# Kernel optimization log

Hardware: AMD Instinct MI355X
Metric: run time of the kernel (lower is better)

Reference implementation:

```python
import jax, jax.numpy as jnp
import numpy as np

N_USERS = 100000
N_MOVIES = 100000
N_EDGES = 1000000
HIDDEN = 128


def setup_inputs() -> dict:
    key = jax.random.key(0)
    k1, k2, k3, k4, k5, k6, k7 = jax.random.split(key, 7)
    user_features = jax.random.normal(k1, (N_USERS, HIDDEN), dtype=jnp.float32)
    movie_features = jax.random.normal(k2, (N_MOVIES, HIDDEN), dtype=jnp.float32)
    src = jax.random.randint(k3, (N_EDGES,), 0, N_USERS, dtype=jnp.int64 if jax.config.jax_enable_x64 else jnp.int32)
    dst = jax.random.randint(k4, (N_EDGES,), 0, N_MOVIES, dtype=jnp.int64 if jax.config.jax_enable_x64 else jnp.int32)
    edge_index = jnp.stack([src, dst], axis=0)
    # Linear(2*HIDDEN, HIDDEN) params, torch-style init (kaiming uniform ~ U(-1/sqrt(fan_in), 1/sqrt(fan_in)))
    b1_bound = 1.0 / np.sqrt(2 * HIDDEN)
    W1 = jax.random.uniform(k5, (2 * HIDDEN, HIDDEN), minval=-b1_bound, maxval=b1_bound, dtype=jnp.float32)
    b1 = jax.random.uniform(k6, (HIDDEN,), minval=-b1_bound, maxval=b1_bound, dtype=jnp.float32)
    b2_bound = 1.0 / np.sqrt(HIDDEN)
    k8, k9 = jax.random.split(k7)
    W2 = jax.random.uniform(k8, (HIDDEN, 1), minval=-b2_bound, maxval=b2_bound, dtype=jnp.float32)
    b2 = jax.random.uniform(k9, (1,), minval=-b2_bound, maxval=b2_bound, dtype=jnp.float32)
    return {"user_features": user_features, "movie_features": movie_features,
            "edge_index": edge_index, "W1": W1, "b1": b1, "W2": W2, "b2": b2}


def reference(user_features, movie_features, edge_index, W1, b1, W2, b2):
    # Gather endpoint features per edge: [E, H] each
    u = user_features[edge_index[0]]
    m = movie_features[edge_index[1]]
    edge_feats = jnp.concatenate([u, m], axis=1)  # [E, 2H]
    h = jax.nn.relu(edge_feats @ W1 + b1)         # [E, H]
    out = h @ W2 + b2                             # [E, 1]
    return out.reshape(-1)
```

## Files before the change

### kernel.cpp

```cpp
#include <hip/hip_runtime.h>
#include <hip/hip_bf16.h>

typedef short s8v __attribute__((ext_vector_type(8)));
typedef float f4v __attribute__((ext_vector_type(4)));

__device__ __forceinline__ unsigned int bfround(float f) {
    unsigned int x = __float_as_uint(f);
    return (x + 0x7fffu + ((x >> 16) & 1u)) >> 16;
}
__device__ __forceinline__ unsigned int pkbf(float x, float y) {
    __hip_bfloat162 h = __float22bfloat162_rn(make_float2(x, y));
    return *(unsigned int*)&h;
}
__device__ __forceinline__ float i8f(unsigned int w, int k) {
    return (float)((int)(signed char)(w >> (8 * k)));
}

__global__ __launch_bounds__(256) void pack_w(const float* __restrict__ W1,
                                              uint4* __restrict__ WF)
{
    const int half = blockIdx.x;
    #pragma unroll
    for (int iter = 0; iter < 8; ++iter) {
        int idx  = iter * 256 + threadIdx.x;
        int lane = idx & 63;
        int t    = (idx >> 6) & 7;
        int c    = idx >> 9;
        int q = lane >> 4, m = lane & 15;
        unsigned int w[4];
        #pragma unroll
        for (int jj = 0; jj < 4; ++jj) {
            float lo = W1[(size_t)(half * 128 + c * 32 + q * 8 + 2 * jj    ) * 128 + t * 16 + m];
            float hi = W1[(size_t)(half * 128 + c * 32 + q * 8 + 2 * jj + 1) * 128 + t * 16 + m];
            w[jj] = bfround(lo) | (bfround(hi) << 16);
        }
        WF[(size_t)half * 2048 + idx] = make_uint4(w[0], w[1], w[2], w[3]);
    }
}

__global__ __launch_bounds__(256, 2) void proj_kernel(
    const float* __restrict__ userf, const float* __restrict__ movief,
    const uint4* __restrict__ WF, const float* __restrict__ b1,
    uint2* __restrict__ Pu, uint2* __restrict__ Pm,
    float* __restrict__ SU, float* __restrict__ SM,
    int ntiles, int bph)
{
    const int half = blockIdx.x >= bph;
    const int bid  = half ? blockIdx.x - bph : blockIdx.x;
    const float* __restrict__ feat = half ? movief : userf;
    uint2* __restrict__ P = half ? Pm : Pu;
    float* __restrict__ S = half ? SM : SU;
    const uint4* __restrict__ wfh = WF + (size_t)half * 2048;

    const int lane = threadIdx.x & 63;
    const int m    = lane & 15;
    const int q    = lane >> 4;

    s8v bfrag[8][4];
    #pragma unroll
    for (int c = 0; c < 4; ++c)
        #pragma unroll
        for (int t = 0; t < 8; ++t) {
            uint4 f = wfh[(c * 8 + t) * 64 + lane];
            bfrag[t][c] = *(const s8v*)&f;
        }

    float bias_v[8];
    #pragma unroll
    for (int t = 0; t < 8; ++t)
        bias_v[t] = half ? b1[t * 16 + m] : 0.0f;

    const int wid = bid * 4 + (threadIdx.x >> 6);
    const int nw  = bph * 4;

#define LOAD_A(dst, t_) do {                                            \
        const float4* arow_ = (const float4*)feat + (size_t)(t_) * 512; \
        _Pragma("unroll")                                               \
        for (int c_ = 0; c_ < 4; ++c_) {                                \
            dst[c_][0] = arow_[m * 32 + c_ * 8 + q * 2 + 0];            \
            dst[c_][1] = arow_[m * 32 + c_ * 8 + q * 2 + 1];            \
        }                                                               \
    } while (0)

    float4 a[4][2];
    int tile = wid;
    if (tile < ntiles) LOAD_A(a, tile);

    while (tile < ntiles) {
        const int nxt = tile + nw;
        float4 an[4][2];
        if (nxt < ntiles) LOAD_A(an, nxt);

        f4v acc[8];
        #pragma unroll
        for (int t = 0; t < 8; ++t)
            acc[t] = (f4v){bias_v[t], bias_v[t], bias_v[t], bias_v[t]};

        #pragma unroll
        for (int c = 0; c < 4; ++c) {
            uint4 aw;
            aw.x = pkbf(a[c][0].x, a[c][0].y);
            aw.y = pkbf(a[c][0].z, a[c][0].w);
            aw.z = pkbf(a[c][1].x, a[c][1].y);
            aw.w = pkbf(a[c][1].z, a[c][1].w);
            s8v af = *(const s8v*)&aw;

            #pragma unroll
            for (int t = 0; t < 8; ++t)
                acc[t] = __builtin_amdgcn_mfma_f32_16x16x32_bf16(af, bfrag[t][c], acc[t], 0, 0, 0);
        }

        #pragma unroll
        for (int r = 0; r < 4; ++r) {
            float mx = 0.0f;
            #pragma unroll
            for (int t = 0; t < 8; ++t) mx = fmaxf(mx, fabsf(acc[t][r]));
            #pragma unroll
            for (int off = 1; off < 16; off <<= 1)
                mx = fmaxf(mx, __shfl_xor(mx, off, 64));
            float inv = mx > 0.0f ? 127.0f / mx : 0.0f;

            unsigned int lo = 0, hi = 0;
            #pragma unroll
            for (int t = 0; t < 4; ++t) {
                lo |= ((unsigned int)(__float2int_rn(acc[t][r]     * inv) & 0xff)) << (8 * t);
                hi |= ((unsigned int)(__float2int_rn(acc[t + 4][r] * inv) & 0xff)) << (8 * t);
            }
            int row = tile * 16 + q * 4 + r;
            P[(size_t)row * 16 + m] = make_uint2(lo, hi);
            if (m == 0) S[row] = mx * (1.0f / 127.0f);
        }

        #pragma unroll
        for (int c = 0; c < 4; ++c) {
            a[c][0] = an[c][0];
            a[c][1] = an[c][1];
        }
        tile = nxt;
    }
#undef LOAD_A
}

__global__ __launch_bounds__(256) void edge_kernel(
    const int* __restrict__ src, const int* __restrict__ dst,
    const uint2* __restrict__ Pu, const uint2* __restrict__ Pm,
    const float* __restrict__ SU, const float* __restrict__ SM,
    const float* __restrict__ W2, const float* __restrict__ b2,
    float* __restrict__ out)
{
    const int lane = threadIdx.x & 63;
    const int L    = lane & 15;
    const int g    = lane >> 4;
    const int eg   = (blockIdx.x * 4 + (threadIdx.x >> 6)) * 16 + g * 4;

    float w2v[8];
    #pragma unroll
    for (int j = 0; j < 8; ++j) w2v[j] = W2[j * 16 + L];

    int si[4], di[4];
    #pragma unroll
    for (int i = 0; i < 4; ++i) { si[i] = src[eg + i]; di[i] = dst[eg + i]; }

    uint2 pu[4], pm[4];
    float scu[4], scm[4];
    #pragma unroll
    for (int i = 0; i < 4; ++i) {
        pu[i] = Pu[(size_t)si[i] * 16 + L];
        pm[i] = Pm[(size_t)di[i] * 16 + L];
        scu[i] = SU[si[i]];
        scm[i] = SM[di[i]];
    }

    float res[4];
    #pragma unroll
    for (int i = 0; i < 4; ++i) {
        const unsigned int uw[2] = {pu[i].x, pu[i].y};
        const unsigned int mw[2] = {pm[i].x, pm[i].y};
        float acc = 0.0f;
        #pragma unroll
        for (int v = 0; v < 2; ++v) {
            #pragma unroll
            for (int k = 0; k < 4; ++k) {
                float h = fmaf(scu[i], i8f(uw[v], k), scm[i] * i8f(mw[v], k));
                acc = fmaf(fmaxf(h, 0.0f), w2v[v * 4 + k], acc);
            }
        }
        #pragma unroll
        for (int off = 1; off < 16; off <<= 1)
            acc += __shfl_xor(acc, off, 64);
        res[i] = acc;
    }

    if (L == 0) {
        float bb = b2[0];
        *(float4*)(out + eg) = make_float4(res[0] + bb, res[1] + bb, res[2] + bb, res[3] + bb);
    }
}

extern "C" void kernel_launch(void* const* d_in, const int* in_sizes, int n_in,
                              void* d_out, int out_size, void* d_ws, size_t ws_size,
                              hipStream_t stream) {
    const float* userf  = (const float*)d_in[0];
    const float* movief = (const float*)d_in[1];
    const int*   eidx   = (const int*)d_in[2];
    const float* W1     = (const float*)d_in[3];
    const float* b1     = (const float*)d_in[4];
    const float* W2     = (const float*)d_in[5];
    const float* b2     = (const float*)d_in[6];
    float* out = (float*)d_out;

    const int NU = in_sizes[0] / 128;
    const int NM = in_sizes[1] / 128;
    const int E  = in_sizes[2] / 2;

    uint2* Pu = (uint2*)d_ws;
    uint2* Pm = Pu + (size_t)NU * 16;
    float* SU = (float*)(Pm + (size_t)NM * 16);
    float* SM = SU + NU;
    uint4* WF = (uint4*)(SM + NM);

    const int ntiles = NU / 16;
    const int bph    = 512;

    pack_w<<<2, 256, 0, stream>>>(W1, WF);
    proj_kernel<<<2 * bph, 256, 0, stream>>>(userf, movief, WF, b1, Pu, Pm, SU, SM, ntiles, bph);
    edge_kernel<<<E / 64, 256, 0, stream>>>(eidx, eidx + E, Pu, Pm, SU, SM, W2, b2, out);
}
```

Baseline: 188.1 us.

## Stage W1 fragments in LDS and raise proj_kernel occupancy

The bf16 weight fragments move out of per-thread registers (128 VGPRs) into a 32KB shared-memory buffer that each block fills once and then reads inside the MFMA loop. The next tile's activations are converted to bf16 right after loading instead of being copied between register arrays. With fewer registers, launch bounds rise from 2 to 4 blocks per CU so more waves can hide the global-load latency of the memory-bound projection. The trade is extra LDS reads on every tile and a block-wide sync at startup.

```diff
diff --git a/kernel.cpp b/kernel.cpp
--- a/kernel.cpp
+++ b/kernel.cpp
@@ -38,13 +38,15 @@
     }
 }
 
-__global__ __launch_bounds__(256, 2) void proj_kernel(
+__global__ __launch_bounds__(256, 4) void proj_kernel(
     const float* __restrict__ userf, const float* __restrict__ movief,
     const uint4* __restrict__ WF, const float* __restrict__ b1,
     uint2* __restrict__ Pu, uint2* __restrict__ Pm,
     float* __restrict__ SU, float* __restrict__ SM,
     int ntiles, int bph)
 {
+    __shared__ uint4 wlds[2048];
+
     const int half = blockIdx.x >= bph;
     const int bid  = half ? blockIdx.x - bph : blockIdx.x;
     const float* __restrict__ feat = half ? movief : userf;
@@ -52,18 +54,14 @@
     float* __restrict__ S = half ? SM : SU;
     const uint4* __restrict__ wfh = WF + (size_t)half * 2048;
 
+    #pragma unroll
+    for (int i = 0; i < 8; ++i)
+        wlds[i * 256 + threadIdx.x] = wfh[i * 256 + threadIdx.x];
+    __syncthreads();
+
     const int lane = threadIdx.x & 63;
     const int m    = lane & 15;
     const int q    = lane >> 4;
-
-    s8v bfrag[8][4];
-    #pragma unroll
-    for (int c = 0; c < 4; ++c)
-        #pragma unroll
-        for (int t = 0; t < 8; ++t) {
-            uint4 f = wfh[(c * 8 + t) * 64 + lane];
-            bfrag[t][c] = *(const s8v*)&f;
-        }
 
     float bias_v[8];
     #pragma unroll
@@ -82,13 +80,28 @@
         }                                                               \
     } while (0)
 
-    float4 a[4][2];
+#define CVT_A() do {                                                    \
+        _Pragma("unroll")                                               \
+        for (int c_ = 0; c_ < 4; ++c_) {                                \
+            uint4 aw_;                                                  \
+            aw_.x = pkbf(an[c_][0].x, an[c_][0].y);                     \
+            aw_.y = pkbf(an[c_][0].z, an[c_][0].w);                     \
+            aw_.z = pkbf(an[c_][1].x, an[c_][1].y);                     \
+            aw_.w = pkbf(an[c_][1].z, an[c_][1].w);                     \
+            af[c_] = *(const s8v*)&aw_;                                 \
+        }                                                               \
+    } while (0)
+
+    float4 an[4][2];
+    s8v    af[4];
     int tile = wid;
-    if (tile < ntiles) LOAD_A(a, tile);
+    if (tile < ntiles) {
+        LOAD_A(an, tile);
+        CVT_A();
+    }
 
     while (tile < ntiles) {
         const int nxt = tile + nw;
-        float4 an[4][2];
         if (nxt < ntiles) LOAD_A(an, nxt);
 
         f4v acc[8];
@@ -98,16 +111,11 @@
 
         #pragma unroll
         for (int c = 0; c < 4; ++c) {
-            uint4 aw;
-            aw.x = pkbf(a[c][0].x, a[c][0].y);
-            aw.y = pkbf(a[c][0].z, a[c][0].w);
-            aw.z = pkbf(a[c][1].x, a[c][1].y);
-            aw.w = pkbf(a[c][1].z, a[c][1].w);
-            s8v af = *(const s8v*)&aw;
-
-            #pragma unroll
-            for (int t = 0; t < 8; ++t)
-                acc[t] = __builtin_amdgcn_mfma_f32_16x16x32_bf16(af, bfrag[t][c], acc[t], 0, 0, 0);
+            #pragma unroll
+            for (int t = 0; t < 8; ++t) {
+                uint4 f = wlds[(c * 8 + t) * 64 + lane];
+                acc[t] = __builtin_amdgcn_mfma_f32_16x16x32_bf16(af[c], *(const s8v*)&f, acc[t], 0, 0, 0);
+            }
         }
 
         #pragma unroll
@@ -131,14 +139,11 @@
             if (m == 0) S[row] = mx * (1.0f / 127.0f);
         }
 
-        #pragma unroll
-        for (int c = 0; c < 4; ++c) {
-            a[c][0] = an[c][0];
-            a[c][1] = an[c][1];
-        }
+        if (nxt < ntiles) CVT_A();
         tile = nxt;
     }
 #undef LOAD_A
+#undef CVT_A
 }
 
 __global__ __launch_bounds__(256) void edge_kernel(
```

After: 293.9 us. +56.2%, slower.
